# Kernel tuning notes

Measured on AMD Instinct MI355X. Metric: run time of the kernel, lower is better.

The kernel has to match this reference:

```python
import jax, jax.numpy as jnp
import numpy as np

N_ADAPTERS = 16
RANK = 16
ALPHA = 16.0
SCALING = ALPHA / RANK
B, S, IN, OUT = 32, 512, 1024, 4096


def setup_inputs() -> dict:
    key = jax.random.key(0)
    k1, k2, k3, k4, k5, k6 = jax.random.split(key, 6)
    hidden_states = jax.random.normal(k1, (B, S, IN), dtype=jnp.float32)
    adapter_ids = jax.random.randint(k2, (B,), 0, N_ADAPTERS, dtype=jnp.int64)
    W = jax.random.normal(k3, (IN, OUT), dtype=jnp.float32) * 0.02
    b = jax.random.normal(k4, (OUT,), dtype=jnp.float32) * 0.02
    lora_a = jax.random.normal(k5, (N_ADAPTERS, IN, RANK), dtype=jnp.float32) * (1.0 / np.sqrt(IN))
    lora_b = jax.random.normal(k6, (N_ADAPTERS, RANK, OUT), dtype=jnp.float32) * 0.02
    return {"hidden_states": hidden_states, "adapter_ids": adapter_ids,
            "W": W, "b": b, "lora_a": lora_a, "lora_b": lora_b}


def reference(hidden_states, adapter_ids, W, b, lora_a, lora_b):
    # Base Conv1D (GPT-2 style): x @ W + b  -> [B, S, OUT]
    base_output = jnp.einsum('bsi,io->bso', hidden_states, W) + b
    # Per-sample adapter gather (replaces the unique-id loop + boolean masks):
    a_sel = lora_a[adapter_ids]          # [B, IN, R]
    b_sel = lora_b[adapter_ids]          # [B, R, OUT]
    low_rank = jnp.einsum('bsi,bir->bsr', hidden_states, a_sel)   # [B, S, R]
    delta = jnp.einsum('bsr,bro->bso', low_rank, b_sel) * SCALING # [B, S, OUT]
    return base_output + delta
```

## Files before the change

### kernel.cpp

```cpp
#include <hip/hip_runtime.h>

#define M_TOT 16384
#define N_TOT 4096
#define K_TOT 1024
#define R_LORA 16

#define BM 256
#define BN 256
#define BK 64
#define NSTEP 64

typedef __attribute__((ext_vector_type(8))) short bf16x8_t;
typedef __attribute__((ext_vector_type(4))) float f32x4_t;

__device__ __forceinline__ unsigned short f2bf(float f) {
  unsigned u = __builtin_bit_cast(unsigned, f);
  u += 0x7FFFu + ((u >> 16) & 1u);
  return (unsigned short)(u >> 16);
}

__device__ __forceinline__ void gload_lds16(const void* g, void* l) {
  __builtin_amdgcn_global_load_lds(
      (const __attribute__((address_space(1))) unsigned int*)g,
      (__attribute__((address_space(3))) unsigned int*)l, 16, 0, 0);
}

__global__ __launch_bounds__(256) void prep_kernel(const float* __restrict__ x,
                                                   const float* __restrict__ W,
                                                   const float* __restrict__ lora_a,
                                                   const float* __restrict__ lora_b,
                                                   unsigned short* __restrict__ xB,
                                                   unsigned short* __restrict__ WtB,
                                                   unsigned short* __restrict__ AtB,
                                                   unsigned short* __restrict__ lbT) {
  __shared__ float lds[64][65];
  const int bid = blockIdx.x;
  const int t = threadIdx.x;
  if (bid < 1024) {
    size_t i = (size_t)bid * 256 + t;
    const size_t stride = (size_t)1024 * 256;
    const size_t n4 = (size_t)M_TOT * K_TOT / 4;
    for (; i < n4; i += stride) {
      float4 v = ((const float4*)x)[i];
      ushort4 h;
      h.x = f2bf(v.x); h.y = f2bf(v.y); h.z = f2bf(v.z); h.w = f2bf(v.w);
      ((ushort4*)xB)[i] = h;
    }
  } else if (bid < 2048) {
    const int v = bid - 1024;
    const int k0 = (v & 15) * 64;
    const int n0 = (v >> 4) * 64;
    const int rr = t >> 4;
    const int cc = (t & 15) * 4;
#pragma unroll
    for (int i = 0; i < 4; ++i) {
      int row = i * 16 + rr;
      float4 w4 = *(const float4*)(W + (size_t)(k0 + row) * N_TOT + n0 + cc);
      lds[row][cc + 0] = w4.x; lds[row][cc + 1] = w4.y;
      lds[row][cc + 2] = w4.z; lds[row][cc + 3] = w4.w;
    }
    __syncthreads();
#pragma unroll
    for (int i = 0; i < 4; ++i) {
      int nrow = i * 16 + rr;
      ushort4 h;
      h.x = f2bf(lds[cc + 0][nrow]); h.y = f2bf(lds[cc + 1][nrow]);
      h.z = f2bf(lds[cc + 2][nrow]); h.w = f2bf(lds[cc + 3][nrow]);
      *(ushort4*)(WtB + (size_t)(n0 + nrow) * K_TOT + k0 + cc) = h;
    }
  } else {
    const int b2 = bid - 2048;
    if (b2 < 64) {
      int idx = b2 * 256 + t;
      int aid = idx >> 10;
      int k = idx & 1023;
      const float* src = lora_a + (size_t)idx * 16;
#pragma unroll
      for (int q = 0; q < 4; ++q) {
        float4 v4 = ((const float4*)src)[q];
#pragma unroll
        for (int j = 0; j < 4; ++j) {
          int r = q * 4 + j;
          float val = (j == 0) ? v4.x : (j == 1) ? v4.y : (j == 2) ? v4.z : v4.w;
          AtB[(((size_t)aid * 16 + r) << 10) + k] = f2bf(val);
        }
      }
    } else {
      int idx = (b2 - 64) * 256 + t;
      int aid = idx >> 12;
      int n = idx & 4095;
      unsigned short o[16];
#pragma unroll
      for (int r = 0; r < 16; ++r)
        o[r] = f2bf(lora_b[((size_t)aid * 16 + r) * N_TOT + n]);
      ushort4* dst = (ushort4*)(lbT + ((size_t)aid * N_TOT + n) * 16);
#pragma unroll
      for (int q = 0; q < 4; ++q) {
        ushort4 h; h.x = o[q*4+0]; h.y = o[q*4+1]; h.z = o[q*4+2]; h.w = o[q*4+3];
        dst[q] = h;
      }
    }
  }
}

__global__ __launch_bounds__(256) void lowrank_kernel(const unsigned short* __restrict__ xB,
                                                      const unsigned short* __restrict__ AtB,
                                                      const int* __restrict__ aids,
                                                      unsigned short* __restrict__ lrB) {
  __shared__ char As[128 * 128];
  const int blk = blockIdx.x;
  const int t = threadIdx.x;
  const int lane = t & 63;
  const int w = t >> 6;
  const int fr = lane & 15, fq = lane >> 4;
  const int aid = aids[blk >> 2];

  const unsigned short* aSrc[4];
  char* aDst[4];
#pragma unroll
  for (int r = 0; r < 4; ++r) {
    int off = (r * 256 + t) * 16;
    int row = off >> 7, cb = off & 127;
    int sb = cb ^ ((row & 7) << 4);
    aSrc[r] = xB + (size_t)(blk * 128 + row) * K_TOT + (sb >> 1);
    aDst[r] = As + off;
  }
  const unsigned short* bBase = AtB + ((size_t)aid * 16 + fr) * K_TOT + fq * 8;

  f32x4_t acc[2];
  acc[0] = (f32x4_t){0.f, 0.f, 0.f, 0.f};
  acc[1] = (f32x4_t){0.f, 0.f, 0.f, 0.f};

  for (int kt = 0; kt < K_TOT / 64; ++kt) {
#pragma unroll
    for (int r = 0; r < 4; ++r) gload_lds16(aSrc[r] + kt * 64, aDst[r]);
    __syncthreads();
#pragma unroll
    for (int ks = 0; ks < 2; ++ks) {
      bf16x8_t bfr = *(const bf16x8_t*)(bBase + kt * 64 + ks * 32);
#pragma unroll
      for (int m = 0; m < 2; ++m) {
        int row = w * 32 + m * 16 + fr;
        int cb = ks * 64 + fq * 16;
        bf16x8_t af = *(const bf16x8_t*)(As + row * 128 + (cb ^ ((row & 7) << 4)));
        acc[m] = __builtin_amdgcn_mfma_f32_16x16x32_bf16(af, bfr, acc[m], 0, 0, 0);
      }
    }
    __syncthreads();
  }
#pragma unroll
  for (int m = 0; m < 2; ++m) {
    int gm0 = blk * 128 + w * 32 + m * 16 + fq * 4;
#pragma unroll
    for (int q = 0; q < 4; ++q)
      lrB[(size_t)(gm0 + q) * R_LORA + fr] = f2bf(acc[m][q]);
  }
}

#define BAR() __builtin_amdgcn_s_barrier()
#define WAIT_LGKM0() asm volatile("s_waitcnt lgkmcnt(0)" ::: "memory")

#define STAGE_HALF(gbase, koff, ldsbase)                                   \
  do {                                                                     \
    gload_lds16((const char*)(gbase) + (koff), (ldsbase) + t * 16);        \
    gload_lds16((const char*)(gbase) + 64 * 2048 + (koff),                 \
                (ldsbase) + 8192 + t * 16);                                \
  } while (0)

#define LDA(MH)                                                            \
  do {                                                                     \
    _Pragma("unroll") for (int m = 0; m < 4; ++m)                          \
      _Pragma("unroll") for (int ks = 0; ks < 2; ++ks)                     \
        aF[m][ks] = *(const bf16x8_t*)(bufA + (MH) * 8192 + m * 2048 +     \
                                       (laneA ^ (ks << 6)));               \
  } while (0)

#define LDB(NH)                                                            \
  do {                                                                     \
    _Pragma("unroll") for (int n = 0; n < 2; ++n)                          \
      _Pragma("unroll") for (int ks = 0; ks < 2; ++ks)                     \
        bF[NH][n][ks] = *(const bf16x8_t*)(bufB + (NH) * 4096 + n * 2048 + \
                                           (laneA ^ (ks << 6)));           \
  } while (0)

#define MM(MH, NH)                                                         \
  do {                                                                     \
    __builtin_amdgcn_s_setprio(1);                                         \
    _Pragma("unroll") for (int ks = 0; ks < 2; ++ks)                       \
      _Pragma("unroll") for (int m = 0; m < 4; ++m)                        \
        _Pragma("unroll") for (int n = 0; n < 2; ++n)                      \
          acc[(MH) * 4 + m][(NH) * 2 + n] =                                \
              __builtin_amdgcn_mfma_f32_16x16x32_bf16(                     \
                  aF[m][ks], bF[NH][n][ks],                                \
                  acc[(MH) * 4 + m][(NH) * 2 + n], 0, 0, 0);               \
    __builtin_amdgcn_s_setprio(0);                                         \
  } while (0)

__global__ __launch_bounds__(512, 2) void gemm_kernel(
    const unsigned short* __restrict__ xB, const unsigned short* __restrict__ WtB,
    const unsigned short* __restrict__ lrB, const unsigned short* __restrict__ lbT,
    const float* __restrict__ bias, const int* __restrict__ aids,
    float* __restrict__ out) {
  __shared__ char smem[131072];

  const int orig = blockIdx.x;
  const int wg = (orig & 7) * 32 + (orig >> 3);
  const int tm = wg & 63;
  const int tn0 = (wg >> 6) * 4;

  const int t = threadIdx.x;
  const int lane = t & 63;
  const int wid = t >> 6;
  const int wr = wid >> 2;
  const int wc = wid & 3;
  const int fr = lane & 15, fq = lane >> 4;

  const int laneA = fr * 128 + (((fq << 4) ^ ((fr & 7) << 4)));
  const int waveAoff = wr * 16384;
  const int waveBoff = 32768 + (wc >> 1) * 16384 + (wc & 1) * 8192;

  const int srow = t >> 3;
  const int sb = (((t & 7) ^ (srow & 7)) << 4);
  const char* pAsrc0 = (const char*)xB + (size_t)(tm * 256 + srow) * 2048 + sb;
  const char* pAsrc1 = pAsrc0 + (size_t)128 * 2048;
  const char* pBbase = (const char*)WtB + (size_t)srow * 2048 + sb;

  f32x4_t acc[8][4];
#pragma unroll
  for (int m = 0; m < 8; ++m)
#pragma unroll
    for (int n = 0; n < 4; ++n) acc[m][n] = (f32x4_t){0.f, 0.f, 0.f, 0.f};

  bf16x8_t aF[4][2];
  bf16x8_t bF[2][2][2];

  {
    const char* pB0 = pBbase + (size_t)tn0 * 256 * 2048;
    STAGE_HALF(pAsrc0, 0, smem + 0);
    STAGE_HALF(pAsrc1, 0, smem + 16384);
    STAGE_HALF(pB0, 0, smem + 32768);
    STAGE_HALF(pB0 + (size_t)128 * 2048, 0, smem + 49152);
    STAGE_HALF(pB0, 128, smem + 65536 + 32768);
    STAGE_HALF(pB0 + (size_t)128 * 2048, 128, smem + 65536 + 49152);
  }
  asm volatile("s_waitcnt vmcnt(4)" ::: "memory");
  BAR();

#pragma unroll 1
  for (int s = 0; s < NSTEP; ++s) {
    char* base = smem + ((s & 1) << 16);
    char* nbase = smem + (((s + 1) & 1) << 16);
    char* bufA = base + waveAoff;
    char* bufB = base + waveBoff;
    const int ka1 = ((s + 1) & 15) * 128;
    const bool stA = (s + 1 < NSTEP);
    const bool stB = (s + 2 < NSTEP);
    const char* pBs = pBbase;
    int kb2 = 0;
    if (stB) {
      int s2 = s + 2;
      pBs = pBbase + (size_t)(tn0 + (s2 >> 4)) * 256 * 2048;
      kb2 = (s2 & 15) * 128;
    }

    LDA(0);
    LDB(0);
    if (stA) STAGE_HALF(pAsrc0, ka1, nbase + 0);
    asm volatile("s_waitcnt lgkmcnt(8)" ::: "memory");
    BAR(); WAIT_LGKM0();
    MM(0, 0);
    BAR();

    LDB(1);
    if (stA) STAGE_HALF(pAsrc1, ka1, nbase + 16384);
    BAR(); WAIT_LGKM0();
    MM(0, 1);
    BAR();

    LDA(1);
    if (stB) STAGE_HALF(pBs, kb2, base + 32768);
    BAR(); WAIT_LGKM0();
    MM(1, 1);
    BAR();

    if (stB) STAGE_HALF(pBs + (size_t)128 * 2048, kb2, base + 49152);
    BAR(); WAIT_LGKM0();
    MM(1, 0);
    if (s < NSTEP - 2) asm volatile("s_waitcnt vmcnt(4)" ::: "memory");
    else               asm volatile("s_waitcnt vmcnt(0)" ::: "memory");
    BAR();

    if ((s & 15) == 15) {
      const int j = s >> 4;
      const int tn = tn0 + j;
      const int aid = aids[tm >> 1];
      bf16x8_t z8 = (bf16x8_t){0, 0, 0, 0, 0, 0, 0, 0};
      bf16x8_t lrf[8], lbf[4];
#pragma unroll
      for (int m = 0; m < 8; ++m) lrf[m] = z8;
#pragma unroll
      for (int n = 0; n < 4; ++n) lbf[n] = z8;
      if (fq < 2) {
#pragma unroll
        for (int m = 0; m < 8; ++m)
          lrf[m] = *(const bf16x8_t*)(lrB + (size_t)(tm * 256 + wr * 128 + m * 16 + fr) * R_LORA + fq * 8);
#pragma unroll
        for (int n = 0; n < 4; ++n)
          lbf[n] = *(const bf16x8_t*)(lbT + ((size_t)aid * N_TOT + tn * 256 + wc * 64 + n * 16 + fr) * R_LORA + fq * 8);
      }
#pragma unroll
      for (int m = 0; m < 8; ++m)
#pragma unroll
        for (int n = 0; n < 4; ++n)
          acc[m][n] = __builtin_amdgcn_mfma_f32_16x16x32_bf16(lrf[m], lbf[n], acc[m][n], 0, 0, 0);

#pragma unroll
      for (int n = 0; n < 4; ++n) {
        int gn = tn * 256 + wc * 64 + n * 16 + fr;
        float bv = bias[gn];
#pragma unroll
        for (int m = 0; m < 8; ++m) {
          int gm0 = tm * 256 + wr * 128 + m * 16 + fq * 4;
          float* op = out + (size_t)gm0 * N_TOT + gn;
#pragma unroll
          for (int q = 0; q < 4; ++q) op[(size_t)q * N_TOT] = acc[m][n][q] + bv;
        }
      }
#pragma unroll
      for (int m = 0; m < 8; ++m)
#pragma unroll
        for (int n = 0; n < 4; ++n) acc[m][n] = (f32x4_t){0.f, 0.f, 0.f, 0.f};
    }
  }
}

extern "C" void kernel_launch(void* const* d_in, const int* in_sizes, int n_in,
                              void* d_out, int out_size, void* d_ws, size_t ws_size,
                              hipStream_t stream) {
  const float* x      = (const float*)d_in[0];
  const int*   aids   = (const int*)d_in[1];
  const float* W      = (const float*)d_in[2];
  const float* bias   = (const float*)d_in[3];
  const float* lora_a = (const float*)d_in[4];
  const float* lora_b = (const float*)d_in[5];
  float* out = (float*)d_out;

  char* ws = (char*)d_ws;
  unsigned short* xB  = (unsigned short*)(ws);
  unsigned short* WtB = (unsigned short*)(ws + (size_t)32 * 1024 * 1024);
  unsigned short* lrB = (unsigned short*)(ws + (size_t)40 * 1024 * 1024);
  unsigned short* AtB = (unsigned short*)(ws + (size_t)40 * 1024 * 1024 + 512 * 1024);
  unsigned short* lbT = (unsigned short*)(ws + (size_t)41 * 1024 * 1024);

  prep_kernel<<<2368, 256, 0, stream>>>(x, W, lora_a, lora_b, xB, WtB, AtB, lbT);
  lowrank_kernel<<<128, 256, 0, stream>>>(xB, AtB, aids, lrB);
  gemm_kernel<<<256, 512, 0, stream>>>(xB, WtB, lrB, lbT, bias, aids, out);
}
```

Baseline: 240.1 us.

## Keep W panel resident per block and sweep four M tiles instead of N

Each persistent block now owns a single N tile of W and walks four consecutive M tiles, where before it owned one M tile and walked four N tiles. The block ID to tile mapping is rearranged so each XCD handles two N panels, which is meant to raise L2 reuse of W and spread x traffic differently. The epilogue now selects the per-tile adapter from the changing M tile. W is re-streamed on each M pass, so the gain depends on L2 hit behaviour across XCDs.

```diff
diff --git a/kernel.cpp b/kernel.cpp
--- a/kernel.cpp
+++ b/kernel.cpp
@@ -204,9 +204,10 @@
   __shared__ char smem[131072];
 
   const int orig = blockIdx.x;
-  const int wg = (orig & 7) * 32 + (orig >> 3);
-  const int tm = wg & 63;
-  const int tn0 = (wg >> 6) * 4;
+  const int xcd = orig & 7;
+  const int j = orig >> 3;
+  const int tn = xcd * 2 + (j & 1);
+  const int tmg = j >> 1;
 
   const int t = threadIdx.x;
   const int lane = t & 63;
@@ -221,9 +222,8 @@
 
   const int srow = t >> 3;
   const int sb = (((t & 7) ^ (srow & 7)) << 4);
-  const char* pAsrc0 = (const char*)xB + (size_t)(tm * 256 + srow) * 2048 + sb;
-  const char* pAsrc1 = pAsrc0 + (size_t)128 * 2048;
-  const char* pBbase = (const char*)WtB + (size_t)srow * 2048 + sb;
+  const char* pAbase = (const char*)xB + (size_t)(tmg * 1024 + srow) * 2048 + sb;
+  const char* pBpanel = (const char*)WtB + (size_t)(tn * 256 + srow) * 2048 + sb;
 
   f32x4_t acc[8][4];
 #pragma unroll
@@ -234,15 +234,12 @@
   bf16x8_t aF[4][2];
   bf16x8_t bF[2][2][2];
 
-  {
-    const char* pB0 = pBbase + (size_t)tn0 * 256 * 2048;
-    STAGE_HALF(pAsrc0, 0, smem + 0);
-    STAGE_HALF(pAsrc1, 0, smem + 16384);
-    STAGE_HALF(pB0, 0, smem + 32768);
-    STAGE_HALF(pB0 + (size_t)128 * 2048, 0, smem + 49152);
-    STAGE_HALF(pB0, 128, smem + 65536 + 32768);
-    STAGE_HALF(pB0 + (size_t)128 * 2048, 128, smem + 65536 + 49152);
-  }
+  STAGE_HALF(pAbase, 0, smem + 0);
+  STAGE_HALF(pAbase + (size_t)128 * 2048, 0, smem + 16384);
+  STAGE_HALF(pBpanel, 0, smem + 32768);
+  STAGE_HALF(pBpanel + (size_t)128 * 2048, 0, smem + 49152);
+  STAGE_HALF(pBpanel, 128, smem + 65536 + 32768);
+  STAGE_HALF(pBpanel + (size_t)128 * 2048, 128, smem + 65536 + 49152);
   asm volatile("s_waitcnt vmcnt(4)" ::: "memory");
   BAR();
 
@@ -252,38 +249,37 @@
     char* nbase = smem + (((s + 1) & 1) << 16);
     char* bufA = base + waveAoff;
     char* bufB = base + waveBoff;
-    const int ka1 = ((s + 1) & 15) * 128;
-    const bool stA = (s + 1 < NSTEP);
-    const bool stB = (s + 2 < NSTEP);
-    const char* pBs = pBbase;
-    int kb2 = 0;
-    if (stB) {
-      int s2 = s + 2;
-      pBs = pBbase + (size_t)(tn0 + (s2 >> 4)) * 256 * 2048;
-      kb2 = (s2 & 15) * 128;
-    }
+
+    const int u1 = s + 1;
+    const bool stA = (u1 < NSTEP);
+    const char* pA1 = pAbase + (size_t)(u1 >> 4) * (256 * 2048);
+    const int ka1 = (u1 & 15) * 128;
+
+    const int u2 = s + 2;
+    const bool stB = (u2 < NSTEP);
+    const int kb2 = (u2 & 15) * 128;
 
     LDA(0);
     LDB(0);
-    if (stA) STAGE_HALF(pAsrc0, ka1, nbase + 0);
+    if (stA) STAGE_HALF(pA1, ka1, nbase + 0);
     asm volatile("s_waitcnt lgkmcnt(8)" ::: "memory");
     BAR(); WAIT_LGKM0();
     MM(0, 0);
     BAR();
 
     LDB(1);
-    if (stA) STAGE_HALF(pAsrc1, ka1, nbase + 16384);
+    if (stA) STAGE_HALF(pA1 + (size_t)128 * 2048, ka1, nbase + 16384);
     BAR(); WAIT_LGKM0();
     MM(0, 1);
     BAR();
 
     LDA(1);
-    if (stB) STAGE_HALF(pBs, kb2, base + 32768);
+    if (stB) STAGE_HALF(pBpanel, kb2, base + 32768);
     BAR(); WAIT_LGKM0();
     MM(1, 1);
     BAR();
 
-    if (stB) STAGE_HALF(pBs + (size_t)128 * 2048, kb2, base + 49152);
+    if (stB) STAGE_HALF(pBpanel + (size_t)128 * 2048, kb2, base + 49152);
     BAR(); WAIT_LGKM0();
     MM(1, 0);
     if (s < NSTEP - 2) asm volatile("s_waitcnt vmcnt(4)" ::: "memory");
@@ -291,8 +287,7 @@
     BAR();
 
     if ((s & 15) == 15) {
-      const int j = s >> 4;
-      const int tn = tn0 + j;
+      const int tm = tmg * 4 + (s >> 4);
       const int aid = aids[tm >> 1];
       bf16x8_t z8 = (bf16x8_t){0, 0, 0, 0, 0, 0, 0, 0};
       bf16x8_t lrf[8], lbf[4];
```

Result: faster. 214.5 us (-10.7%).
